# Kernel optimization log

Hardware: AMD Instinct MI355X
Metric: run time of the kernel (lower is better)

Reference implementation:

```python
import jax, jax.numpy as jnp
import numpy as np
import math

B, S, D, H = 4, 2048, 1024, 16
DH = D // H  # 64


def setup_inputs() -> dict:
    key = jax.random.key(0)
    ks = jax.random.split(key, 7)
    scale = 1.0 / math.sqrt(D)
    q = jax.random.normal(ks[0], (B, S, D), dtype=jnp.float32)
    k = jax.random.normal(ks[1], (B, S, D), dtype=jnp.float32)
    v = jax.random.normal(ks[2], (B, S, D), dtype=jnp.float32)
    mask = jnp.tril(jnp.ones((S, S), dtype=jnp.int32))[None, None]  # [1,1,S,S] causal
    wq = jax.random.normal(ks[3], (D, D), dtype=jnp.float32) * scale
    wk = jax.random.normal(ks[4], (D, D), dtype=jnp.float32) * scale
    wv = jax.random.normal(ks[5], (D, D), dtype=jnp.float32) * scale
    wo = jax.random.normal(ks[6], (D, D), dtype=jnp.float32) * scale
    return {"q": q, "k": k, "v": v, "mask": mask, "wq": wq, "wk": wk, "wv": wv, "wo": wo}


def reference(q, k, v, mask, wq, wk, wv, wo):
    # nn.Linear(bias=False): y = x @ W.T
    qry = q @ wq.T
    key = k @ wk.T
    val = v @ wv.T
    # [B,S,D] -> [B,H,S,DH]
    qry = qry.reshape(B, S, H, DH).transpose(0, 2, 1, 3)
    key = key.reshape(B, S, H, DH).transpose(0, 2, 1, 3)
    val = val.reshape(B, S, H, DH).transpose(0, 2, 1, 3)
    scores = jnp.einsum('bhqd,bhkd->bhqk', qry, key) / math.sqrt(DH)
    scores = jnp.where(mask == 0, jnp.float32(-1e9), scores)
    attn = jax.nn.softmax(scores, axis=-1)  # dropout p=0.0 -> identity
    x = jnp.einsum('bhqk,bhkd->bhqd', attn, val)
    x = x.transpose(0, 2, 1, 3).reshape(B, S, D)
    return x @ wo.T
```

## Files before the change

### kernel.cpp

```cpp
#include <hip/hip_runtime.h>
#include <hip/hip_bf16.h>

typedef __attribute__((ext_vector_type(8))) short bf16x8;
typedef __attribute__((ext_vector_type(4))) float f32x4;
typedef __attribute__((ext_vector_type(16))) float f32x16;

#define MFMA16(a, b, c) __builtin_amdgcn_mfma_f32_16x16x32_bf16((a), (b), (c), 0, 0, 0)
#define MFMA32(a, b, c) __builtin_amdgcn_mfma_f32_32x32x16_bf16((a), (b), (c), 0, 0, 0)

__device__ __forceinline__ short f2b(float f) {
  unsigned u = __builtin_bit_cast(unsigned, f);
  u += 0x7FFFu + ((u >> 16) & 1u);
  return (short)(u >> 16);
}
__device__ __forceinline__ unsigned cvtpk(float lo, float hi) {
  unsigned r;
  asm("v_cvt_pk_bf16_f32 %0, %1, %2" : "=v"(r) : "v"(lo), "v"(hi));
  return r;
}

__global__ __launch_bounds__(256) void cvt_bf16(const float* __restrict__ s,
                                                short* __restrict__ d, int n8) {
  int i = blockIdx.x * 256 + threadIdx.x;
  if (i >= n8) return;
  const float4* sp = (const float4*)s;
  float4 a = sp[2 * i], b = sp[2 * i + 1];
  bf16x8 o;
  o[0] = f2b(a.x); o[1] = f2b(a.y); o[2] = f2b(a.z); o[3] = f2b(a.w);
  o[4] = f2b(b.x); o[5] = f2b(b.y); o[6] = f2b(b.z); o[7] = f2b(b.w);
  *(bf16x8*)(d + (long)i * 8) = o;
}

template <int MODE>
__global__ __launch_bounds__(256) void gemm_bt(const short* __restrict__ A,
                                               const short* __restrict__ BT,
                                               void* __restrict__ Cout,
                                               int M, int N, int K, float oscale) {
  __shared__ __align__(16) short As[128 * 64];
  __shared__ __align__(16) short Bs[128 * 64];
  const int t = threadIdx.x;
  const int l = t & 63, w = t >> 6;
  const int grp = l >> 4, li = l & 15;
  const int nbn = N >> 7;
  const int bm = (int)blockIdx.x / nbn, bn = (int)blockIdx.x % nbn;
  const int m0 = bm << 7, n0 = bn << 7;
  const int wm = (w >> 1) << 6, wn = (w & 1) << 6;
  const int srow = t >> 3, scol = (t & 7) << 3;
  f32x4 acc[4][4] = {};
  for (int kt = 0; kt < K; kt += 64) {
#pragma unroll
    for (int i = 0; i < 4; ++i) {
      const short* ga = A + (long)(m0 + i * 32 + srow) * K + kt + scol;
      __builtin_amdgcn_global_load_lds(
          (const __attribute__((address_space(1))) void*)ga,
          (__attribute__((address_space(3))) void*)&As[i * 2048 + t * 8], 16, 0, 0);
    }
#pragma unroll
    for (int i = 0; i < 4; ++i) {
      const short* gb = BT + (long)(n0 + i * 32 + srow) * K + kt + scol;
      __builtin_amdgcn_global_load_lds(
          (const __attribute__((address_space(1))) void*)gb,
          (__attribute__((address_space(3))) void*)&Bs[i * 2048 + t * 8], 16, 0, 0);
    }
    __syncthreads();
#pragma unroll
    for (int kk = 0; kk < 64; kk += 32) {
      bf16x8 af[4], bfr[4];
#pragma unroll
      for (int mi = 0; mi < 4; ++mi)
        af[mi] = *(const bf16x8*)&As[(wm + mi * 16 + li) * 64 + kk + grp * 8];
#pragma unroll
      for (int ni = 0; ni < 4; ++ni)
        bfr[ni] = *(const bf16x8*)&Bs[(wn + ni * 16 + li) * 64 + kk + grp * 8];
#pragma unroll
      for (int mi = 0; mi < 4; ++mi)
#pragma unroll
        for (int ni = 0; ni < 4; ++ni)
          acc[mi][ni] = MFMA16(af[mi], bfr[ni], acc[mi][ni]);
    }
    __syncthreads();
  }
#pragma unroll
  for (int mi = 0; mi < 4; ++mi) {
#pragma unroll
    for (int ni = 0; ni < 4; ++ni) {
      f32x4 v = acc[mi][ni];
      int n = n0 + wn + ni * 16 + li;
#pragma unroll
      for (int r = 0; r < 4; ++r) {
        int m = m0 + wm + mi * 16 + grp * 4 + r;
        if (MODE == 2) {
          ((float*)Cout)[(long)m * N + n] = v[r];
        } else {
          int b = m >> 11, sq = m & 2047;
          int h = n >> 6, dh = n & 63;
          if (MODE == 0)
            ((short*)Cout)[(((long)(b * 16 + h) * 2048 + sq) << 6) + dh] = f2b(v[r] * oscale);
          else
            ((short*)Cout)[(((long)(b * 16 + h) * 64 + dh) << 11) + sq] = f2b(v[r] * oscale);
        }
      }
    }
  }
}

__global__ __launch_bounds__(256) void attn_fwd(const short* __restrict__ Qh,
                                                const short* __restrict__ Kh,
                                                const short* __restrict__ Vt,
                                                short* __restrict__ Xb) {
  __shared__ __align__(16) short Ks[2][4096];
  __shared__ __align__(16) short Vs[2][4096];
  const int bh = blockIdx.x;
  const int qt = 15 - (int)blockIdx.y;
  const int t = threadIdx.x, l = t & 63, w = t >> 6;
  const int q = l & 31, hi = l >> 5;
  const int q0w = qt * 128 + w * 32;
  const int qg = q0w + q;
  const short* Qp = Qh + (long)bh * 131072;
  const char* Kb = (const char*)(Kh + (long)bh * 131072);
  const char* Vb = (const char*)(Vt + (long)bh * 131072);

  bf16x8 qf[4];
#pragma unroll
  for (int kd = 0; kd < 4; ++kd)
    qf[kd] = *(const bf16x8*)(Qp + (long)qg * 64 + kd * 16 + hi * 8);

  const int co0 = t * 16, co1 = co0 + 4096;

  f32x16 oa = {}, ob = {};
  float mrun = -1e30f, lsum = 0.f;
  const int myTrips = (q0w >> 6) + 1;
  const int nt = 2 * qt + 2;

#define STAGE(KT, BUF)                                                                   \
  {                                                                                      \
    long ktb = (long)(KT) * 8192;                                                        \
    _Pragma("unroll") for (int c = 0; c < 2; ++c) {                                      \
      int o = c ? co1 : co0;                                                             \
      int ksrc = o ^ (((o >> 7) & 7) << 4);                                              \
      __builtin_amdgcn_global_load_lds(                                                  \
          (const __attribute__((address_space(1))) void*)(Kb + ktb + ksrc),              \
          (__attribute__((address_space(3))) void*)((char*)Ks[BUF] + o), 16, 0, 0);      \
      int row = o >> 7, c16 = (o >> 4) & 7;                                              \
      int vsrc = row * 4096 + (KT) * 128 + (((c16 ^ (row & 7))) << 4);                   \
      __builtin_amdgcn_global_load_lds(                                                  \
          (const __attribute__((address_space(1))) void*)(Vb + vsrc),                    \
          (__attribute__((address_space(3))) void*)((char*)Vs[BUF] + o), 16, 0, 0);      \
    }                                                                                    \
  }

  STAGE(0, 0);
  __syncthreads();

  for (int kt = 0; kt < nt; ++kt) {
    const int buf = kt & 1;
    if (kt + 1 < nt) STAGE(kt + 1, buf ^ 1);

    if (kt < myTrips) {
      const bool diag = (kt == myTrips - 1);
      const int khmax = (diag && ((q0w & 32) == 0)) ? 1 : 2;

      f32x16 p0 = {}, p1 = {};
#pragma unroll
      for (int kd = 0; kd < 4; ++kd) {
        int colB = kd * 32 + hi * 16;
        bf16x8 kf0 = *(const bf16x8*)((const char*)Ks[buf] + q * 128 + (colB ^ ((q & 7) << 4)));
        p0 = MFMA32(kf0, qf[kd], p0);
      }
      if (khmax == 2) {
#pragma unroll
        for (int kd = 0; kd < 4; ++kd) {
          int colB = kd * 32 + hi * 16;
          bf16x8 kf1 = *(const bf16x8*)((const char*)Ks[buf] + (q + 32) * 128 + (colB ^ ((q & 7) << 4)));
          p1 = MFMA32(kf1, qf[kd], p1);
        }
      }
      if (diag) {
#pragma unroll
        for (int r = 0; r < 16; ++r) {
          int key0 = kt * 64 + (r & 3) + 8 * (r >> 2) + 4 * hi;
          if (key0 > qg) p0[r] = -1e30f;
          if (key0 + 32 > qg) p1[r] = -1e30f;
        }
      }
      float pm = p0[0];
#pragma unroll
      for (int r = 1; r < 16; ++r) pm = fmaxf(pm, p0[r]);
      if (khmax == 2) {
#pragma unroll
        for (int r = 0; r < 16; ++r) pm = fmaxf(pm, p1[r]);
      }
      pm = fmaxf(pm, __shfl_xor(pm, 32));
      float mn = fmaxf(mrun, pm);
      float alpha = __expf(mrun - mn);
      mrun = mn;
      float ts = 0.f;
#pragma unroll
      for (int r = 0; r < 16; ++r) { p0[r] = __expf(p0[r] - mn); ts += p0[r]; }
      if (khmax == 2) {
#pragma unroll
        for (int r = 0; r < 16; ++r) { p1[r] = __expf(p1[r] - mn); ts += p1[r]; }
      }
      ts += __shfl_xor(ts, 32);
      lsum = lsum * alpha + ts;
#pragma unroll
      for (int r = 0; r < 16; ++r) { oa[r] *= alpha; ob[r] *= alpha; }

      unsigned own0[8], prt0[8], own1[8], prt1[8];
#pragma unroll
      for (int g = 0; g < 4; ++g) {
        own0[2 * g]     = cvtpk(p0[4 * g], p0[4 * g + 1]);
        own0[2 * g + 1] = cvtpk(p0[4 * g + 2], p0[4 * g + 3]);
      }
#pragma unroll
      for (int i = 0; i < 8; ++i) prt0[i] = __shfl_xor(own0[i], 32);
      if (khmax == 2) {
#pragma unroll
        for (int g = 0; g < 4; ++g) {
          own1[2 * g]     = cvtpk(p1[4 * g], p1[4 * g + 1]);
          own1[2 * g + 1] = cvtpk(p1[4 * g + 2], p1[4 * g + 3]);
        }
#pragma unroll
        for (int i = 0; i < 8; ++i) prt1[i] = __shfl_xor(own1[i], 32);
      }

#define PVSTEP(KD, OWN, PRT)                                                              \
      {                                                                                   \
        const int kdl = (KD) & 1;                                                         \
        unsigned b0 = hi ? PRT[4 * kdl + 2] : OWN[4 * kdl];                               \
        unsigned b1 = hi ? PRT[4 * kdl + 3] : OWN[4 * kdl + 1];                           \
        unsigned b2 = hi ? OWN[4 * kdl + 2] : PRT[4 * kdl];                               \
        unsigned b3 = hi ? OWN[4 * kdl + 3] : PRT[4 * kdl + 1];                           \
        int4 bi = {(int)b0, (int)b1, (int)b2, (int)b3};                                   \
        bf16x8 pb = __builtin_bit_cast(bf16x8, bi);                                       \
        int colB = (KD) * 32 + hi * 16;                                                   \
        bf16x8 vf0 = *(const bf16x8*)((const char*)Vs[buf] + q * 128 + (colB ^ ((q & 7) << 4)));          \
        bf16x8 vf1 = *(const bf16x8*)((const char*)Vs[buf] + (q + 32) * 128 + (colB ^ ((q & 7) << 4)));   \
        oa = MFMA32(vf0, pb, oa);                                                         \
        ob = MFMA32(vf1, pb, ob);                                                         \
      }
      PVSTEP(0, own0, prt0);
      PVSTEP(1, own0, prt0);
      if (khmax == 2) {
        PVSTEP(2, own1, prt1);
        PVSTEP(3, own1, prt1);
      }
#undef PVSTEP
    }
    __syncthreads();
  }

  const float inv = 1.f / lsum;
  const int b = bh >> 4, h = bh & 15;
  short* orow = Xb + (long)(b * 2048 + qg) * 1024 + h * 64;
#pragma unroll
  for (int g = 0; g < 4; ++g) {
    {
      unsigned u0 = cvtpk(oa[4 * g] * inv, oa[4 * g + 1] * inv);
      unsigned u1 = cvtpk(oa[4 * g + 2] * inv, oa[4 * g + 3] * inv);
      uint2 uu = {u0, u1};
      *(uint2*)(orow + 8 * g + 4 * hi) = uu;
    }
    {
      unsigned u0 = cvtpk(ob[4 * g] * inv, ob[4 * g + 1] * inv);
      unsigned u1 = cvtpk(ob[4 * g + 2] * inv, ob[4 * g + 3] * inv);
      uint2 uu = {u0, u1};
      *(uint2*)(orow + 32 + 8 * g + 4 * hi) = uu;
    }
  }
}

extern "C" void kernel_launch(void* const* d_in, const int* in_sizes, int n_in,
                              void* d_out, int out_size, void* d_ws, size_t ws_size,
                              hipStream_t stream) {
  const float* q  = (const float*)d_in[0];
  const float* k  = (const float*)d_in[1];
  const float* v  = (const float*)d_in[2];
  const float* wq = (const float*)d_in[4];
  const float* wk = (const float*)d_in[5];
  const float* wv = (const float*)d_in[6];
  const float* wo = (const float*)d_in[7];

  short* ws = (short*)d_ws;
  const long T = 8388608;
  short* qb  = ws;
  short* kb  = qb + T;
  short* vb  = kb + T;
  short* Qh  = vb + T;
  short* Kh  = Qh + T;
  short* Vt  = Kh + T;
  short* Xb  = Vt + T;
  short* wqb = Xb + T;
  short* wkb = wqb + 1048576;
  short* wvb = wkb + 1048576;
  short* wob = wvb + 1048576;

  cvt_bf16<<<4096, 256, 0, stream>>>(q, qb, 1048576);
  cvt_bf16<<<4096, 256, 0, stream>>>(k, kb, 1048576);
  cvt_bf16<<<4096, 256, 0, stream>>>(v, vb, 1048576);
  cvt_bf16<<<512, 256, 0, stream>>>(wq, wqb, 131072);
  cvt_bf16<<<512, 256, 0, stream>>>(wk, wkb, 131072);
  cvt_bf16<<<512, 256, 0, stream>>>(wv, wvb, 131072);
  cvt_bf16<<<512, 256, 0, stream>>>(wo, wob, 131072);

  gemm_bt<0><<<512, 256, 0, stream>>>(qb, wqb, (void*)Qh, 8192, 1024, 1024, 0.125f);
  gemm_bt<0><<<512, 256, 0, stream>>>(kb, wkb, (void*)Kh, 8192, 1024, 1024, 1.0f);
  gemm_bt<1><<<512, 256, 0, stream>>>(vb, wvb, (void*)Vt, 8192, 1024, 1024, 1.0f);
  attn_fwd<<<dim3(64, 16), 256, 0, stream>>>(Qh, Kh, Vt, Xb);
  gemm_bt<2><<<512, 256, 0, stream>>>(Xb, wob, d_out, 8192, 1024, 1024, 1.0f);
}
```

Measured before the change: 240.7 us.

## Pair causal query tiles per block, use exp2 softmax with lazy rescaling

Each attention block now processes two query tiles, qt and 15-qt, so every block does the same amount of causal work. Both tiles reuse the same staged K/V tiles, which halves the grid and the K/V loads per query. The softmax now uses exp2, with log2(e) folded into the Q scale, and skips the running-max rescale when the new max exceeds the old by less than a threshold. It also adds s_setprio around the MFMA sections and launch_bounds(256,2). The cost is higher register pressure from two sets of accumulators, and the skipped rescale relies on the threshold keeping fp32 values bounded.

Measured after the change: 223.8 us. -7.0%, faster.

```diff
diff --git a/kernel.cpp b/kernel.cpp
--- a/kernel.cpp
+++ b/kernel.cpp
@@ -7,6 +7,15 @@
 
 #define MFMA16(a, b, c) __builtin_amdgcn_mfma_f32_16x16x32_bf16((a), (b), (c), 0, 0, 0)
 #define MFMA32(a, b, c) __builtin_amdgcn_mfma_f32_32x32x16_bf16((a), (b), (c), 0, 0, 0)
+
+#if defined(__has_builtin)
+#if __has_builtin(__builtin_amdgcn_exp2f)
+#define EXP2(x) __builtin_amdgcn_exp2f(x)
+#endif
+#endif
+#ifndef EXP2
+#define EXP2(x) exp2f(x)
+#endif
 
 __device__ __forceinline__ short f2b(float f) {
   unsigned u = __builtin_bit_cast(unsigned, f);
@@ -104,33 +113,142 @@
   }
 }
 
-__global__ __launch_bounds__(256) void attn_fwd(const short* __restrict__ Qh,
-                                                const short* __restrict__ Kh,
-                                                const short* __restrict__ Vt,
-                                                short* __restrict__ Xb) {
+__device__ __forceinline__ void attn_tile(const short* Kbuf, const short* Vbuf,
+                                          const bf16x8 qf[4], f32x16& oa, f32x16& ob,
+                                          float& mrun, float& lsum, int kt, bool diag,
+                                          int khmax, int qg, int q, int hi) {
+  f32x16 p0 = {}, p1 = {};
+  __builtin_amdgcn_s_setprio(1);
+#pragma unroll
+  for (int kd = 0; kd < 4; ++kd) {
+    int colB = kd * 32 + hi * 16;
+    bf16x8 kf0 = *(const bf16x8*)((const char*)Kbuf + q * 128 + (colB ^ ((q & 7) << 4)));
+    p0 = MFMA32(kf0, qf[kd], p0);
+  }
+  if (khmax == 2) {
+#pragma unroll
+    for (int kd = 0; kd < 4; ++kd) {
+      int colB = kd * 32 + hi * 16;
+      bf16x8 kf1 = *(const bf16x8*)((const char*)Kbuf + (q + 32) * 128 + (colB ^ ((q & 7) << 4)));
+      p1 = MFMA32(kf1, qf[kd], p1);
+    }
+  }
+  __builtin_amdgcn_s_setprio(0);
+  if (diag) {
+#pragma unroll
+    for (int r = 0; r < 16; ++r) {
+      int key0 = kt * 64 + (r & 3) + 8 * (r >> 2) + 4 * hi;
+      if (key0 > qg) p0[r] = -1e30f;
+      if (key0 + 32 > qg) p1[r] = -1e30f;
+    }
+  }
+  float pm = p0[0];
+#pragma unroll
+  for (int r = 1; r < 16; ++r) pm = fmaxf(pm, p0[r]);
+  if (khmax == 2) {
+#pragma unroll
+    for (int r = 0; r < 16; ++r) pm = fmaxf(pm, p1[r]);
+  }
+  pm = fmaxf(pm, __shfl_xor(pm, 32));
+  const bool skip = __all(pm - mrun <= 11.5f);
+  float mn;
+  float alpha = 1.f;
+  if (skip) {
+    mn = mrun;
+  } else {
+    mn = fmaxf(mrun, pm);
+    alpha = EXP2(mrun - mn);
+    mrun = mn;
+  }
+  float ts = 0.f;
+#pragma unroll
+  for (int r = 0; r < 16; ++r) { p0[r] = EXP2(p0[r] - mn); ts += p0[r]; }
+  if (khmax == 2) {
+#pragma unroll
+    for (int r = 0; r < 16; ++r) { p1[r] = EXP2(p1[r] - mn); ts += p1[r]; }
+  }
+  ts += __shfl_xor(ts, 32);
+  if (skip) {
+    lsum += ts;
+  } else {
+    lsum = lsum * alpha + ts;
+#pragma unroll
+    for (int r = 0; r < 16; ++r) { oa[r] *= alpha; ob[r] *= alpha; }
+  }
+  unsigned own0[8], prt0[8], own1[8], prt1[8];
+#pragma unroll
+  for (int g = 0; g < 4; ++g) {
+    own0[2 * g]     = cvtpk(p0[4 * g], p0[4 * g + 1]);
+    own0[2 * g + 1] = cvtpk(p0[4 * g + 2], p0[4 * g + 3]);
+  }
+#pragma unroll
+  for (int i = 0; i < 8; ++i) prt0[i] = __shfl_xor(own0[i], 32);
+  if (khmax == 2) {
+#pragma unroll
+    for (int g = 0; g < 4; ++g) {
+      own1[2 * g]     = cvtpk(p1[4 * g], p1[4 * g + 1]);
+      own1[2 * g + 1] = cvtpk(p1[4 * g + 2], p1[4 * g + 3]);
+    }
+#pragma unroll
+    for (int i = 0; i < 8; ++i) prt1[i] = __shfl_xor(own1[i], 32);
+  }
+  __builtin_amdgcn_s_setprio(1);
+#define PVSTEP(KD, OWN, PRT)                                                              \
+  {                                                                                       \
+    const int kdl = (KD) & 1;                                                             \
+    unsigned b0 = hi ? PRT[4 * kdl + 2] : OWN[4 * kdl];                                   \
+    unsigned b1 = hi ? PRT[4 * kdl + 3] : OWN[4 * kdl + 1];                               \
+    unsigned b2 = hi ? OWN[4 * kdl + 2] : PRT[4 * kdl];                                   \
+    unsigned b3 = hi ? OWN[4 * kdl + 3] : PRT[4 * kdl + 1];                               \
+    int4 bi = {(int)b0, (int)b1, (int)b2, (int)b3};                                       \
+    bf16x8 pb = __builtin_bit_cast(bf16x8, bi);                                           \
+    int colB = (KD) * 32 + hi * 16;                                                       \
+    bf16x8 vf0 = *(const bf16x8*)((const char*)Vbuf + q * 128 + (colB ^ ((q & 7) << 4))); \
+    bf16x8 vf1 = *(const bf16x8*)((const char*)Vbuf + (q + 32) * 128 + (colB ^ ((q & 7) << 4))); \
+    oa = MFMA32(vf0, pb, oa);                                                             \
+    ob = MFMA32(vf1, pb, ob);                                                             \
+  }
+  PVSTEP(0, own0, prt0);
+  PVSTEP(1, own0, prt0);
+  if (khmax == 2) {
+    PVSTEP(2, own1, prt1);
+    PVSTEP(3, own1, prt1);
+  }
+#undef PVSTEP
+  __builtin_amdgcn_s_setprio(0);
+}
+
+__global__ __launch_bounds__(256, 2) void attn_fwd(const short* __restrict__ Qh,
+                                                   const short* __restrict__ Kh,
+                                                   const short* __restrict__ Vt,
+                                                   short* __restrict__ Xb) {
   __shared__ __align__(16) short Ks[2][4096];
   __shared__ __align__(16) short Vs[2][4096];
   const int bh = blockIdx.x;
-  const int qt = 15 - (int)blockIdx.y;
+  const int qtA = blockIdx.y;
+  const int qtB = 15 - qtA;
   const int t = threadIdx.x, l = t & 63, w = t >> 6;
   const int q = l & 31, hi = l >> 5;
-  const int q0w = qt * 128 + w * 32;
-  const int qg = q0w + q;
+  const int q0wA = qtA * 128 + w * 32, q0wB = qtB * 128 + w * 32;
+  const int qgA = q0wA + q, qgB = q0wB + q;
   const short* Qp = Qh + (long)bh * 131072;
   const char* Kb = (const char*)(Kh + (long)bh * 131072);
   const char* Vb = (const char*)(Vt + (long)bh * 131072);
 
-  bf16x8 qf[4];
-#pragma unroll
-  for (int kd = 0; kd < 4; ++kd)
-    qf[kd] = *(const bf16x8*)(Qp + (long)qg * 64 + kd * 16 + hi * 8);
+  bf16x8 qfA[4], qfB[4];
+#pragma unroll
+  for (int kd = 0; kd < 4; ++kd) {
+    qfA[kd] = *(const bf16x8*)(Qp + (long)qgA * 64 + kd * 16 + hi * 8);
+    qfB[kd] = *(const bf16x8*)(Qp + (long)qgB * 64 + kd * 16 + hi * 8);
+  }
 
   const int co0 = t * 16, co1 = co0 + 4096;
 
-  f32x16 oa = {}, ob = {};
-  float mrun = -1e30f, lsum = 0.f;
-  const int myTrips = (q0w >> 6) + 1;
-  const int nt = 2 * qt + 2;
+  f32x16 oaA = {}, obA = {}, oaB = {}, obB = {};
+  float mrunA = -1e30f, lsumA = 0.f, mrunB = -1e30f, lsumB = 0.f;
+  const int tripsA = (q0wA >> 6) + 1;
+  const int tripsB = (q0wB >> 6) + 1;
+  const int nt = 2 * qtB + 2;
 
 #define STAGE(KT, BUF)                                                                   \
   {                                                                                      \
@@ -156,118 +274,38 @@
     const int buf = kt & 1;
     if (kt + 1 < nt) STAGE(kt + 1, buf ^ 1);
 
-    if (kt < myTrips) {
-      const bool diag = (kt == myTrips - 1);
-      const int khmax = (diag && ((q0w & 32) == 0)) ? 1 : 2;
-
-      f32x16 p0 = {}, p1 = {};
-#pragma unroll
-      for (int kd = 0; kd < 4; ++kd) {
-        int colB = kd * 32 + hi * 16;
-        bf16x8 kf0 = *(const bf16x8*)((const char*)Ks[buf] + q * 128 + (colB ^ ((q & 7) << 4)));
-        p0 = MFMA32(kf0, qf[kd], p0);
-      }
-      if (khmax == 2) {
-#pragma unroll
-        for (int kd = 0; kd < 4; ++kd) {
-          int colB = kd * 32 + hi * 16;
-          bf16x8 kf1 = *(const bf16x8*)((const char*)Ks[buf] + (q + 32) * 128 + (colB ^ ((q & 7) << 4)));
-          p1 = MFMA32(kf1, qf[kd], p1);
-        }
-      }
-      if (diag) {
-#pragma unroll
-        for (int r = 0; r < 16; ++r) {
-          int key0 = kt * 64 + (r & 3) + 8 * (r >> 2) + 4 * hi;
-          if (key0 > qg) p0[r] = -1e30f;
-          if (key0 + 32 > qg) p1[r] = -1e30f;
-        }
-      }
-      float pm = p0[0];
-#pragma unroll
-      for (int r = 1; r < 16; ++r) pm = fmaxf(pm, p0[r]);
-      if (khmax == 2) {
-#pragma unroll
-        for (int r = 0; r < 16; ++r) pm = fmaxf(pm, p1[r]);
-      }
-      pm = fmaxf(pm, __shfl_xor(pm, 32));
-      float mn = fmaxf(mrun, pm);
-      float alpha = __expf(mrun - mn);
-      mrun = mn;
-      float ts = 0.f;
-#pragma unroll
-      for (int r = 0; r < 16; ++r) { p0[r] = __expf(p0[r] - mn); ts += p0[r]; }
-      if (khmax == 2) {
-#pragma unroll
-        for (int r = 0; r < 16; ++r) { p1[r] = __expf(p1[r] - mn); ts += p1[r]; }
-      }
-      ts += __shfl_xor(ts, 32);
-      lsum = lsum * alpha + ts;
-#pragma unroll
-      for (int r = 0; r < 16; ++r) { oa[r] *= alpha; ob[r] *= alpha; }
-
-      unsigned own0[8], prt0[8], own1[8], prt1[8];
-#pragma unroll
-      for (int g = 0; g < 4; ++g) {
-        own0[2 * g]     = cvtpk(p0[4 * g], p0[4 * g + 1]);
-        own0[2 * g + 1] = cvtpk(p0[4 * g + 2], p0[4 * g + 3]);
-      }
-#pragma unroll
-      for (int i = 0; i < 8; ++i) prt0[i] = __shfl_xor(own0[i], 32);
-      if (khmax == 2) {
-#pragma unroll
-        for (int g = 0; g < 4; ++g) {
-          own1[2 * g]     = cvtpk(p1[4 * g], p1[4 * g + 1]);
-          own1[2 * g + 1] = cvtpk(p1[4 * g + 2], p1[4 * g + 3]);
-        }
-#pragma unroll
-        for (int i = 0; i < 8; ++i) prt1[i] = __shfl_xor(own1[i], 32);
-      }
-
-#define PVSTEP(KD, OWN, PRT)                                                              \
-      {                                                                                   \
-        const int kdl = (KD) & 1;                                                         \
-        unsigned b0 = hi ? PRT[4 * kdl + 2] : OWN[4 * kdl];                               \
-        unsigned b1 = hi ? PRT[4 * kdl + 3] : OWN[4 * kdl + 1];                           \
-        unsigned b2 = hi ? OWN[4 * kdl + 2] : PRT[4 * kdl];                               \
-        unsigned b3 = hi ? OWN[4 * kdl + 3] : PRT[4 * kdl + 1];                           \
-        int4 bi = {(int)b0, (int)b1, (int)b2, (int)b3};                                   \
-        bf16x8 pb = __builtin_bit_cast(bf16x8, bi);                                       \
-        int colB = (KD) * 32 + hi * 16;                                                   \
-        bf16x8 vf0 = *(const bf16x8*)((const char*)Vs[buf] + q * 128 + (colB ^ ((q & 7) << 4)));          \
-        bf16x8 vf1 = *(const bf16x8*)((const char*)Vs[buf] + (q + 32) * 128 + (colB ^ ((q & 7) << 4)));   \
-        oa = MFMA32(vf0, pb, oa);                                                         \
-        ob = MFMA32(vf1, pb, ob);                                                         \
-      }
-      PVSTEP(0, own0, prt0);
-      PVSTEP(1, own0, prt0);
-      if (khmax == 2) {
-        PVSTEP(2, own1, prt1);
-        PVSTEP(3, own1, prt1);
-      }
-#undef PVSTEP
+    if (kt < tripsB) {
+      const bool diag = (kt == tripsB - 1);
+      const int khmax = (diag && ((q0wB & 32) == 0)) ? 1 : 2;
+      attn_tile(Ks[buf], Vs[buf], qfB, oaB, obB, mrunB, lsumB, kt, diag, khmax, qgB, q, hi);
+    }
+    if (kt < tripsA) {
+      const bool diag = (kt == tripsA - 1);
+      const int khmax = (diag && ((q0wA & 32) == 0)) ? 1 : 2;
+      attn_tile(Ks[buf], Vs[buf], qfA, oaA, obA, mrunA, lsumA, kt, diag, khmax, qgA, q, hi);
     }
     __syncthreads();
   }
 
-  const float inv = 1.f / lsum;
   const int b = bh >> 4, h = bh & 15;
-  short* orow = Xb + (long)(b * 2048 + qg) * 1024 + h * 64;
-#pragma unroll
-  for (int g = 0; g < 4; ++g) {
-    {
-      unsigned u0 = cvtpk(oa[4 * g] * inv, oa[4 * g + 1] * inv);
-      unsigned u1 = cvtpk(oa[4 * g + 2] * inv, oa[4 * g + 3] * inv);
-      uint2 uu = {u0, u1};
-      *(uint2*)(orow + 8 * g + 4 * hi) = uu;
-    }
-    {
-      unsigned u0 = cvtpk(ob[4 * g] * inv, ob[4 * g + 1] * inv);
-      unsigned u1 = cvtpk(ob[4 * g + 2] * inv, ob[4 * g + 3] * inv);
-      uint2 uu = {u0, u1};
-      *(uint2*)(orow + 32 + 8 * g + 4 * hi) = uu;
-    }
-  }
+#define EPI(OA, OB, LS, QG)                                                \
+  {                                                                        \
+    const float inv = 1.f / (LS);                                          \
+    short* orow = Xb + (long)(b * 2048 + (QG)) * 1024 + h * 64;            \
+    _Pragma("unroll") for (int g = 0; g < 4; ++g) {                        \
+      unsigned u0 = cvtpk((OA)[4 * g] * inv, (OA)[4 * g + 1] * inv);       \
+      unsigned u1 = cvtpk((OA)[4 * g + 2] * inv, (OA)[4 * g + 3] * inv);   \
+      uint2 uu = {u0, u1};                                                 \
+      *(uint2*)(orow + 8 * g + 4 * hi) = uu;                               \
+      unsigned w0 = cvtpk((OB)[4 * g] * inv, (OB)[4 * g + 1] * inv);       \
+      unsigned w1 = cvtpk((OB)[4 * g + 2] * inv, (OB)[4 * g + 3] * inv);   \
+      uint2 ww = {w0, w1};                                                 \
+      *(uint2*)(orow + 32 + 8 * g + 4 * hi) = ww;                          \
+    }                                                                      \
+  }
+  EPI(oaA, obA, lsumA, qgA);
+  EPI(oaB, obB, lsumB, qgB);
+#undef EPI
 }
 
 extern "C" void kernel_launch(void* const* d_in, const int* in_sizes, int n_in,
@@ -303,9 +341,9 @@
   cvt_bf16<<<512, 256, 0, stream>>>(wv, wvb, 131072);
   cvt_bf16<<<512, 256, 0, stream>>>(wo, wob, 131072);
 
-  gemm_bt<0><<<512, 256, 0, stream>>>(qb, wqb, (void*)Qh, 8192, 1024, 1024, 0.125f);
+  gemm_bt<0><<<512, 256, 0, stream>>>(qb, wqb, (void*)Qh, 8192, 1024, 1024, 0.18033688f);
   gemm_bt<0><<<512, 256, 0, stream>>>(kb, wkb, (void*)Kh, 8192, 1024, 1024, 1.0f);
   gemm_bt<1><<<512, 256, 0, stream>>>(vb, wvb, (void*)Vt, 8192, 1024, 1024, 1.0f);
-  attn_fwd<<<dim3(64, 16), 256, 0, stream>>>(Qh, Kh, Vt, Xb);
+  attn_fwd<<<dim3(64, 8), 256, 0, stream>>>(Qh, Kh, Vt, Xb);
   gemm_bt<2><<<512, 256, 0, stream>>>(Xb, wob, d_out, 8192, 1024, 1024, 1.0f);
 }
```
